# Kernel tuning notes

Measured on AMD Instinct MI355X. Metric: run time of the kernel, lower is better.

Reference implementation:

```python
import jax, jax.numpy as jnp
import numpy as np

B, H, S, D = 8, 12, 1024, 64

def setup_inputs() -> dict:
    key = jax.random.key(0)
    kq, kk, kv = jax.random.split(key, 3)
    q = jax.random.normal(kq, (B, H, S, D), dtype=jnp.float32)
    k = jax.random.normal(kk, (B, H, S, D), dtype=jnp.float32)
    v = jax.random.normal(kv, (B, H, S, D), dtype=jnp.float32)
    scale = 8  # sqrt(d_head)
    return {"q": q, "k": k, "v": v, "scale": scale}

def reference(q, k, v, scale):
    # scores: (B,H,S,S) = q @ k^T / scale, softmax over last axis
    scores = jnp.einsum('bhqd,bhkd->bhqk', q, k) / scale
    attention_score = jax.nn.softmax(scores, axis=-1)
    # context: (B,H,S,D)
    attention_context = jnp.einsum('bhqk,bhkd->bhqd', attention_score, v)
    return (attention_score, attention_context)
```

## Files before the change

kernel.cpp:

```cpp
#include <hip/hip_runtime.h>


#define SLEN 1024
#define DHEAD 64
#define NBH 96

typedef __attribute__((ext_vector_type(4))) float f32x4;
typedef __attribute__((ext_vector_type(8))) __bf16 bf16x8;

#define PL_STRIDE 1032
#define QT_STRIDE 72
#define VT_STRIDE 136

struct SMem {
  __bf16 pl[64][PL_STRIDE];
  union {
    __bf16 qt[64][QT_STRIDE];
    __bf16 vt[64][VT_STRIDE];
  } u;
  float red[8][64];
  float mrow[64];
  float invrow[64];
};

__global__ __launch_bounds__(512, 2)
void attn_fused(const float* __restrict__ Qp, const float* __restrict__ Kp,
                const float* __restrict__ Vp, const int* __restrict__ scale_p,
                float* __restrict__ out) {
  __shared__ SMem sm;
  const int tid  = threadIdx.x;
  const int w    = tid >> 6;
  const int lane = tid & 63;
  const int quad = lane >> 4;
  const int c16  = lane & 15;
  const int bh   = blockIdx.y;
  const int qbase = blockIdx.x * 64;

  int siv = *scale_p;
  float fs = (siv >= 1 && siv <= (1 << 24)) ? (float)siv : __int_as_float(siv);
  const float inv_scale = 1.0f / fs;

  const float* Qg = Qp + ((size_t)bh * SLEN + qbase) * DHEAD;
  const float* Kg = Kp + (size_t)bh * SLEN * DHEAD;
  const float* Vg = Vp + (size_t)bh * SLEN * DHEAD;

  #pragma unroll
  for (int it = 0; it < 2; ++it) {
    int flat = it * 2048 + tid * 4;
    int r = flat >> 6, d = flat & 63;
    f32x4 qv = *(const f32x4*)(Qg + (size_t)r * DHEAD + d);
    #pragma unroll
    for (int j = 0; j < 4; ++j)
      sm.u.qt[r][d + j] = (__bf16)(qv[j] * inv_scale);
  }
  __syncthreads();

  bf16x8 af[4][2];
  #pragma unroll
  for (int rt = 0; rt < 4; ++rt)
    #pragma unroll
    for (int k0 = 0; k0 < 2; ++k0)
      af[rt][k0] = *(const bf16x8*)&sm.u.qt[rt * 16 + c16][k0 * 32 + quad * 8];

  f32x4 acc[4][8];
  {
    f32x4 z = {0.0f, 0.0f, 0.0f, 0.0f};
    #pragma unroll
    for (int rt = 0; rt < 4; ++rt)
      #pragma unroll
      for (int ct = 0; ct < 8; ++ct) acc[rt][ct] = z;
  }

  #pragma unroll
  for (int ct = 0; ct < 8; ++ct) {
    int krow = w * 128 + ct * 16 + c16;
    const float* kr = Kg + (size_t)krow * DHEAD + quad * 8;
    f32x4 k0a = *(const f32x4*)(kr);
    f32x4 k0b = *(const f32x4*)(kr + 4);
    f32x4 k1a = *(const f32x4*)(kr + 32);
    f32x4 k1b = *(const f32x4*)(kr + 36);
    bf16x8 b0, b1;
    #pragma unroll
    for (int j = 0; j < 4; ++j) {
      b0[j]     = (__bf16)k0a[j];
      b0[j + 4] = (__bf16)k0b[j];
      b1[j]     = (__bf16)k1a[j];
      b1[j + 4] = (__bf16)k1b[j];
    }
    #pragma unroll
    for (int rt = 0; rt < 4; ++rt) {
      acc[rt][ct] = __builtin_amdgcn_mfma_f32_16x16x32_bf16(af[rt][0], b0, acc[rt][ct], 0, 0, 0);
      acc[rt][ct] = __builtin_amdgcn_mfma_f32_16x16x32_bf16(af[rt][1], b1, acc[rt][ct], 0, 0, 0);
    }
  }

  float mx[4][4];
  #pragma unroll
  for (int rt = 0; rt < 4; ++rt)
    #pragma unroll
    for (int i = 0; i < 4; ++i) {
      float m = acc[rt][0][i];
      #pragma unroll
      for (int ct = 1; ct < 8; ++ct) m = fmaxf(m, acc[rt][ct][i]);
      mx[rt][i] = m;
    }
  #pragma unroll
  for (int off = 1; off < 16; off <<= 1)
    #pragma unroll
    for (int rt = 0; rt < 4; ++rt)
      #pragma unroll
      for (int i = 0; i < 4; ++i)
        mx[rt][i] = fmaxf(mx[rt][i], __shfl_xor(mx[rt][i], off));
  if (c16 == 0) {
    #pragma unroll
    for (int rt = 0; rt < 4; ++rt)
      #pragma unroll
      for (int i = 0; i < 4; ++i)
        sm.red[w][rt * 16 + quad * 4 + i] = mx[rt][i];
  }
  __syncthreads();
  if (tid < 64) {
    float m = sm.red[0][tid];
    #pragma unroll
    for (int w2 = 1; w2 < 8; ++w2) m = fmaxf(m, sm.red[w2][tid]);
    sm.mrow[tid] = m;
  }
  __syncthreads();

  float sum4[4][4];
  #pragma unroll
  for (int rt = 0; rt < 4; ++rt)
    #pragma unroll
    for (int i = 0; i < 4; ++i) {
      float m = sm.mrow[rt * 16 + quad * 4 + i];
      float s = 0.0f;
      #pragma unroll
      for (int ct = 0; ct < 8; ++ct) {
        float e = __expf(acc[rt][ct][i] - m);
        acc[rt][ct][i] = e;
        s += e;
      }
      sum4[rt][i] = s;
    }
  #pragma unroll
  for (int off = 1; off < 16; off <<= 1)
    #pragma unroll
    for (int rt = 0; rt < 4; ++rt)
      #pragma unroll
      for (int i = 0; i < 4; ++i)
        sum4[rt][i] += __shfl_xor(sum4[rt][i], off);
  if (c16 == 0) {
    #pragma unroll
    for (int rt = 0; rt < 4; ++rt)
      #pragma unroll
      for (int i = 0; i < 4; ++i)
        sm.red[w][rt * 16 + quad * 4 + i] = sum4[rt][i];
  }
  __syncthreads();
  if (tid < 64) {
    float s = 0.0f;
    #pragma unroll
    for (int w2 = 0; w2 < 8; ++w2) s += sm.red[w2][tid];
    sm.invrow[tid] = 1.0f / s;
  }
  __syncthreads();

  const int kap = tid & 127;
  const int dgb = tid >> 7;
  const int scol = (kap & 15) * 8 + (kap >> 4);
  f32x4 pref[4];
  #pragma unroll
  for (int it = 0; it < 4; ++it) {
    int d0 = it * 16 + dgb * 4;
    pref[it] = *(const f32x4*)(Vg + (size_t)kap * DHEAD + d0);
  }

  #pragma unroll
  for (int rt = 0; rt < 4; ++rt) {
    #pragma unroll
    for (int i = 0; i < 4; ++i) {
      int row = rt * 16 + quad * 4 + i;
      float inv = sm.invrow[row];
      float* orow = out + ((size_t)bh * SLEN + qbase + row) * SLEN;
      bf16x8 pk;
      #pragma unroll
      for (int ct = 0; ct < 8; ++ct) {
        float p = acc[rt][ct][i] * inv;
        __builtin_nontemporal_store(p, &orow[w * 128 + ct * 16 + c16]);
        pk[ct] = (__bf16)p;
      }
      *(bf16x8*)&sm.pl[row][w * 128 + c16 * 8] = pk;
    }
  }

  f32x4 ctx[2];
  {
    f32x4 z = {0.0f, 0.0f, 0.0f, 0.0f};
    ctx[0] = z; ctx[1] = z;
  }
  const int prt = w & 3;
  const int dtb = w >> 2;

  for (int sp = 0; sp < 8; ++sp) {
    __syncthreads();
    #pragma unroll
    for (int it = 0; it < 4; ++it) {
      int d0 = it * 16 + dgb * 4;
      #pragma unroll
      for (int j = 0; j < 4; ++j)
        sm.u.vt[d0 + j][scol] = (__bf16)pref[it][j];
    }
    __syncthreads();
    if (sp < 7) {
      #pragma unroll
      for (int it = 0; it < 4; ++it) {
        int d0 = it * 16 + dgb * 4;
        pref[it] = *(const f32x4*)(Vg + (size_t)((sp + 1) * 128 + kap) * DHEAD + d0);
      }
    }
    #pragma unroll
    for (int b2 = 0; b2 < 4; ++b2) {
      bf16x8 a = *(const bf16x8*)&sm.pl[prt * 16 + c16][sp * 128 + b2 * 32 + quad * 8];
      #pragma unroll
      for (int t2 = 0; t2 < 2; ++t2) {
        int dt = dtb + t2 * 2;
        bf16x8 b = *(const bf16x8*)&sm.u.vt[dt * 16 + c16][b2 * 32 + quad * 8];
        ctx[t2] = __builtin_amdgcn_mfma_f32_16x16x32_bf16(a, b, ctx[t2], 0, 0, 0);
      }
    }
  }

  float* outC = out + (size_t)NBH * SLEN * SLEN;
  #pragma unroll
  for (int t2 = 0; t2 < 2; ++t2) {
    int dt = dtb + t2 * 2;
    #pragma unroll
    for (int i = 0; i < 4; ++i) {
      int row = prt * 16 + quad * 4 + i;
      __builtin_nontemporal_store(
          ctx[t2][i],
          &outC[((size_t)bh * SLEN + qbase + row) * DHEAD + dt * 16 + c16]);
    }
  }
}

extern "C" void kernel_launch(void* const* d_in, const int* in_sizes, int n_in,
                              void* d_out, int out_size, void* d_ws, size_t ws_size,
                              hipStream_t stream) {
  (void)in_sizes; (void)n_in; (void)d_ws; (void)ws_size; (void)out_size;
  const float* q = (const float*)d_in[0];
  const float* k = (const float*)d_in[1];
  const float* v = (const float*)d_in[2];
  const int* scale = (const int*)d_in[3];
  float* out = (float*)d_out;
  dim3 grid(SLEN / 64, NBH);
  dim3 block(512);
  hipLaunchKernelGGL(attn_fused, grid, block, 0, stream, q, k, v, scale, out);
}
```

Measured before the change: 645.9 us.

## Shrink query tile to 16 rows, XCD-aware block mapping, direct V loads

Cuts rows per block from 64 to 16 and switches to a 1D grid whose block index is swizzled so all blocks of one (batch, head) land on the same XCD, keeping that head's K/V in the local L2. The PV stage now reads V straight from global memory with double-buffered register prefetch instead of transposing it through LDS. The key range is split across two wave groups whose partial contexts are summed through shared memory. The probability write is moved after the PV matmul and uses plain stores instead of nontemporal ones. In exchange, K and V are re-read four times as often and the strided V loads are uncoalesced, while the smaller LDS footprint allows higher occupancy.

```diff
diff --git a/kernel.cpp b/kernel.cpp
--- a/kernel.cpp
+++ b/kernel.cpp
@@ -4,26 +4,23 @@
 #define SLEN 1024
 #define DHEAD 64
 #define NBH 96
+#define QROWS 16
 
 typedef __attribute__((ext_vector_type(4))) float f32x4;
 typedef __attribute__((ext_vector_type(8))) __bf16 bf16x8;
 
 #define PL_STRIDE 1032
-#define QT_STRIDE 72
-#define VT_STRIDE 136
 
 struct SMem {
-  __bf16 pl[64][PL_STRIDE];
-  union {
-    __bf16 qt[64][QT_STRIDE];
-    __bf16 vt[64][VT_STRIDE];
-  } u;
-  float red[8][64];
-  float mrow[64];
-  float invrow[64];
+  __bf16 pl[QROWS][PL_STRIDE];
+  __bf16 qt[QROWS][72];
+  float red[8][QROWS];
+  float mrow[QROWS];
+  float invrow[QROWS];
+  float ctxr[4][64][4];
 };
 
-__global__ __launch_bounds__(512, 2)
+__global__ __launch_bounds__(512, 4)
 void attn_fused(const float* __restrict__ Qp, const float* __restrict__ Kp,
                 const float* __restrict__ Vp, const int* __restrict__ scale_p,
                 float* __restrict__ out) {
@@ -33,8 +30,12 @@
   const int lane = tid & 63;
   const int quad = lane >> 4;
   const int c16  = lane & 15;
-  const int bh   = blockIdx.y;
-  const int qbase = blockIdx.x * 64;
+
+  const int bid  = blockIdx.x;
+  const int xcd  = bid & 7;
+  const int slot = bid >> 3;
+  const int bh   = xcd * 12 + (slot >> 6);
+  const int qbase = (slot & 63) * QROWS;
 
   int siv = *scale_p;
   float fs = (siv >= 1 && siv <= (1 << 24)) ? (float)siv : __int_as_float(siv);
@@ -44,31 +45,24 @@
   const float* Kg = Kp + (size_t)bh * SLEN * DHEAD;
   const float* Vg = Vp + (size_t)bh * SLEN * DHEAD;
 
-  #pragma unroll
-  for (int it = 0; it < 2; ++it) {
-    int flat = it * 2048 + tid * 4;
-    int r = flat >> 6, d = flat & 63;
+  if (tid < 256) {
+    int r = tid >> 4, d = (tid & 15) * 4;
     f32x4 qv = *(const f32x4*)(Qg + (size_t)r * DHEAD + d);
     #pragma unroll
-    for (int j = 0; j < 4; ++j)
-      sm.u.qt[r][d + j] = (__bf16)(qv[j] * inv_scale);
-  }
-  __syncthreads();
-
-  bf16x8 af[4][2];
-  #pragma unroll
-  for (int rt = 0; rt < 4; ++rt)
-    #pragma unroll
-    for (int k0 = 0; k0 < 2; ++k0)
-      af[rt][k0] = *(const bf16x8*)&sm.u.qt[rt * 16 + c16][k0 * 32 + quad * 8];
-
-  f32x4 acc[4][8];
+    for (int j = 0; j < 4; ++j) sm.qt[r][d + j] = (__bf16)(qv[j] * inv_scale);
+  }
+  __syncthreads();
+
+  bf16x8 af[2];
+  #pragma unroll
+  for (int k0 = 0; k0 < 2; ++k0)
+    af[k0] = *(const bf16x8*)&sm.qt[c16][k0 * 32 + quad * 8];
+
+  f32x4 acc[8];
   {
     f32x4 z = {0.0f, 0.0f, 0.0f, 0.0f};
     #pragma unroll
-    for (int rt = 0; rt < 4; ++rt)
-      #pragma unroll
-      for (int ct = 0; ct < 8; ++ct) acc[rt][ct] = z;
+    for (int ct = 0; ct < 8; ++ct) acc[ct] = z;
   }
 
   #pragma unroll
@@ -87,39 +81,29 @@
       b1[j]     = (__bf16)k1a[j];
       b1[j + 4] = (__bf16)k1b[j];
     }
-    #pragma unroll
-    for (int rt = 0; rt < 4; ++rt) {
-      acc[rt][ct] = __builtin_amdgcn_mfma_f32_16x16x32_bf16(af[rt][0], b0, acc[rt][ct], 0, 0, 0);
-      acc[rt][ct] = __builtin_amdgcn_mfma_f32_16x16x32_bf16(af[rt][1], b1, acc[rt][ct], 0, 0, 0);
-    }
-  }
-
-  float mx[4][4];
-  #pragma unroll
-  for (int rt = 0; rt < 4; ++rt)
-    #pragma unroll
-    for (int i = 0; i < 4; ++i) {
-      float m = acc[rt][0][i];
-      #pragma unroll
-      for (int ct = 1; ct < 8; ++ct) m = fmaxf(m, acc[rt][ct][i]);
-      mx[rt][i] = m;
-    }
+    acc[ct] = __builtin_amdgcn_mfma_f32_16x16x32_bf16(af[0], b0, acc[ct], 0, 0, 0);
+    acc[ct] = __builtin_amdgcn_mfma_f32_16x16x32_bf16(af[1], b1, acc[ct], 0, 0, 0);
+  }
+
+  float mx[4];
+  #pragma unroll
+  for (int i = 0; i < 4; ++i) {
+    float m = acc[0][i];
+    #pragma unroll
+    for (int ct = 1; ct < 8; ++ct) m = fmaxf(m, acc[ct][i]);
+    mx[i] = m;
+  }
   #pragma unroll
   for (int off = 1; off < 16; off <<= 1)
     #pragma unroll
-    for (int rt = 0; rt < 4; ++rt)
-      #pragma unroll
-      for (int i = 0; i < 4; ++i)
-        mx[rt][i] = fmaxf(mx[rt][i], __shfl_xor(mx[rt][i], off));
+    for (int i = 0; i < 4; ++i)
+      mx[i] = fmaxf(mx[i], __shfl_xor(mx[i], off));
   if (c16 == 0) {
     #pragma unroll
-    for (int rt = 0; rt < 4; ++rt)
-      #pragma unroll
-      for (int i = 0; i < 4; ++i)
-        sm.red[w][rt * 16 + quad * 4 + i] = mx[rt][i];
-  }
-  __syncthreads();
-  if (tid < 64) {
+    for (int i = 0; i < 4; ++i) sm.red[w][quad * 4 + i] = mx[i];
+  }
+  __syncthreads();
+  if (tid < QROWS) {
     float m = sm.red[0][tid];
     #pragma unroll
     for (int w2 = 1; w2 < 8; ++w2) m = fmaxf(m, sm.red[w2][tid]);
@@ -127,37 +111,30 @@
   }
   __syncthreads();
 
-  float sum4[4][4];
-  #pragma unroll
-  for (int rt = 0; rt < 4; ++rt)
-    #pragma unroll
-    for (int i = 0; i < 4; ++i) {
-      float m = sm.mrow[rt * 16 + quad * 4 + i];
-      float s = 0.0f;
-      #pragma unroll
-      for (int ct = 0; ct < 8; ++ct) {
-        float e = __expf(acc[rt][ct][i] - m);
-        acc[rt][ct][i] = e;
-        s += e;
-      }
-      sum4[rt][i] = s;
-    }
+  float sum4[4];
+  #pragma unroll
+  for (int i = 0; i < 4; ++i) {
+    float m = sm.mrow[quad * 4 + i];
+    float s = 0.0f;
+    #pragma unroll
+    for (int ct = 0; ct < 8; ++ct) {
+      float e = __expf(acc[ct][i] - m);
+      acc[ct][i] = e;
+      s += e;
+    }
+    sum4[i] = s;
+  }
   #pragma unroll
   for (int off = 1; off < 16; off <<= 1)
     #pragma unroll
-    for (int rt = 0; rt < 4; ++rt)
-      #pragma unroll
-      for (int i = 0; i < 4; ++i)
-        sum4[rt][i] += __shfl_xor(sum4[rt][i], off);
+    for (int i = 0; i < 4; ++i)
+      sum4[i] += __shfl_xor(sum4[i], off);
   if (c16 == 0) {
     #pragma unroll
-    for (int rt = 0; rt < 4; ++rt)
-      #pragma unroll
-      for (int i = 0; i < 4; ++i)
-        sm.red[w][rt * 16 + quad * 4 + i] = sum4[rt][i];
-  }
-  __syncthreads();
-  if (tid < 64) {
+    for (int i = 0; i < 4; ++i) sm.red[w][quad * 4 + i] = sum4[i];
+  }
+  __syncthreads();
+  if (tid < QROWS) {
     float s = 0.0f;
     #pragma unroll
     for (int w2 = 0; w2 < 8; ++w2) s += sm.red[w2][tid];
@@ -165,82 +142,74 @@
   }
   __syncthreads();
 
-  const int kap = tid & 127;
-  const int dgb = tid >> 7;
-  const int scol = (kap & 15) * 8 + (kap >> 4);
-  f32x4 pref[4];
-  #pragma unroll
-  for (int it = 0; it < 4; ++it) {
-    int d0 = it * 16 + dgb * 4;
-    pref[it] = *(const f32x4*)(Vg + (size_t)kap * DHEAD + d0);
-  }
-
-  #pragma unroll
-  for (int rt = 0; rt < 4; ++rt) {
+  #pragma unroll
+  for (int i = 0; i < 4; ++i) {
+    int row = quad * 4 + i;
+    float inv = sm.invrow[row];
+    bf16x8 pk;
+    #pragma unroll
+    for (int ct = 0; ct < 8; ++ct) {
+      float p = acc[ct][i] * inv;
+      acc[ct][i] = p;
+      pk[ct] = (__bf16)p;
+    }
+    *(bf16x8*)&sm.pl[row][w * 128 + c16 * 8] = pk;
+  }
+  __syncthreads();
+
+  const int kpar = w >> 2;
+  const int dt   = w & 3;
+  const float* Vb = Vg + dt * 16 + c16;
+
+  f32x4 ctx = {0.0f, 0.0f, 0.0f, 0.0f};
+  float vr0[8], vr1[8];
+  bf16x8 pa0, pa1;
+
+  auto ldv = [&](float (&dst)[8], int itl) {
+    int kb = (kpar * 4 + (itl >> 2)) * 128 + (itl & 3) * 4 + quad;
+    #pragma unroll
+    for (int j = 0; j < 8; ++j)
+      dst[j] = Vb[(size_t)((kb + j * 16) * DHEAD)];
+  };
+  auto lda = [&](bf16x8& d, int itl) {
+    d = *(const bf16x8*)&sm.pl[c16][(kpar * 4 + (itl >> 2)) * 128 +
+                                    (itl & 3) * 32 + quad * 8];
+  };
+
+  ldv(vr0, 0); lda(pa0, 0);
+  #pragma unroll
+  for (int it = 0; it < 16; it += 2) {
+    ldv(vr1, it + 1); lda(pa1, it + 1);
+    bf16x8 bf0;
+    #pragma unroll
+    for (int j = 0; j < 8; ++j) bf0[j] = (__bf16)vr0[j];
+    ctx = __builtin_amdgcn_mfma_f32_16x16x32_bf16(pa0, bf0, ctx, 0, 0, 0);
+    if (it + 2 < 16) { ldv(vr0, it + 2); lda(pa0, it + 2); }
+    bf16x8 bf1;
+    #pragma unroll
+    for (int j = 0; j < 8; ++j) bf1[j] = (__bf16)vr1[j];
+    ctx = __builtin_amdgcn_mfma_f32_16x16x32_bf16(pa1, bf1, ctx, 0, 0, 0);
+  }
+
+  if (kpar == 1) *(f32x4*)&sm.ctxr[dt][lane][0] = ctx;
+  __syncthreads();
+  if (kpar == 0) {
+    f32x4 o = *(const f32x4*)&sm.ctxr[dt][lane][0];
+    float* outC = out + (size_t)NBH * SLEN * SLEN;
     #pragma unroll
     for (int i = 0; i < 4; ++i) {
-      int row = rt * 16 + quad * 4 + i;
-      float inv = sm.invrow[row];
-      float* orow = out + ((size_t)bh * SLEN + qbase + row) * SLEN;
-      bf16x8 pk;
-      #pragma unroll
-      for (int ct = 0; ct < 8; ++ct) {
-        float p = acc[rt][ct][i] * inv;
-        __builtin_nontemporal_store(p, &orow[w * 128 + ct * 16 + c16]);
-        pk[ct] = (__bf16)p;
-      }
-      *(bf16x8*)&sm.pl[row][w * 128 + c16 * 8] = pk;
-    }
-  }
-
-  f32x4 ctx[2];
-  {
-    f32x4 z = {0.0f, 0.0f, 0.0f, 0.0f};
-    ctx[0] = z; ctx[1] = z;
-  }
-  const int prt = w & 3;
-  const int dtb = w >> 2;
-
-  for (int sp = 0; sp < 8; ++sp) {
-    __syncthreads();
-    #pragma unroll
-    for (int it = 0; it < 4; ++it) {
-      int d0 = it * 16 + dgb * 4;
-      #pragma unroll
-      for (int j = 0; j < 4; ++j)
-        sm.u.vt[d0 + j][scol] = (__bf16)pref[it][j];
-    }
-    __syncthreads();
-    if (sp < 7) {
-      #pragma unroll
-      for (int it = 0; it < 4; ++it) {
-        int d0 = it * 16 + dgb * 4;
-        pref[it] = *(const f32x4*)(Vg + (size_t)((sp + 1) * 128 + kap) * DHEAD + d0);
-      }
-    }
-    #pragma unroll
-    for (int b2 = 0; b2 < 4; ++b2) {
-      bf16x8 a = *(const bf16x8*)&sm.pl[prt * 16 + c16][sp * 128 + b2 * 32 + quad * 8];
-      #pragma unroll
-      for (int t2 = 0; t2 < 2; ++t2) {
-        int dt = dtb + t2 * 2;
-        bf16x8 b = *(const bf16x8*)&sm.u.vt[dt * 16 + c16][b2 * 32 + quad * 8];
-        ctx[t2] = __builtin_amdgcn_mfma_f32_16x16x32_bf16(a, b, ctx[t2], 0, 0, 0);
-      }
-    }
-  }
-
-  float* outC = out + (size_t)NBH * SLEN * SLEN;
-  #pragma unroll
-  for (int t2 = 0; t2 < 2; ++t2) {
-    int dt = dtb + t2 * 2;
-    #pragma unroll
-    for (int i = 0; i < 4; ++i) {
-      int row = prt * 16 + quad * 4 + i;
-      __builtin_nontemporal_store(
-          ctx[t2][i],
-          &outC[((size_t)bh * SLEN + qbase + row) * DHEAD + dt * 16 + c16]);
-    }
+      float r = ctx[i] + o[i];
+      outC[((size_t)bh * SLEN + qbase + quad * 4 + i) * DHEAD + dt * 16 + c16] = r;
+    }
+  }
+
+  #pragma unroll
+  for (int i = 0; i < 4; ++i) {
+    int row = quad * 4 + i;
+    float* orow = out + ((size_t)bh * SLEN + qbase + row) * SLEN;
+    #pragma unroll
+    for (int ct = 0; ct < 8; ++ct)
+      orow[w * 128 + ct * 16 + c16] = acc[ct][i];
   }
 }
 
@@ -253,7 +222,7 @@
   const float* v = (const float*)d_in[2];
   const int* scale = (const int*)d_in[3];
   float* out = (float*)d_out;
-  dim3 grid(SLEN / 64, NBH);
+  dim3 grid((SLEN / QROWS) * NBH);
   dim3 block(512);
   hipLaunchKernelGGL(attn_fused, grid, block, 0, stream, q, k, v, scale, out);
 }
```

After: 693.5 us. 7.4% more time.
